# Performance work log

Measured on AMD Instinct MI355X. Metric: run time of the kernel, lower is better.

## Reference

```python
import jax, jax.numpy as jnp
import numpy as np

N_NODES = 100000
N_EDGES = 1600000
NEG_SLOPE = 0.2  # PyG GATConv default


def setup_inputs() -> dict:
    key = jax.random.key(0)
    ks = jax.random.split(key, 10)
    return {
        "x": jax.random.normal(ks[0], (N_NODES, 128), dtype=jnp.float32),
        "edge_index": jax.random.randint(ks[1], (2, N_EDGES), 0, N_NODES, dtype=jnp.int64),
        "W1": jax.random.normal(ks[2], (128, 128), dtype=jnp.float32) * 0.1,
        "a_src1": jax.random.normal(ks[3], (4, 32), dtype=jnp.float32) * 0.1,
        "a_dst1": jax.random.normal(ks[4], (4, 32), dtype=jnp.float32) * 0.1,
        "b1": jax.random.normal(ks[5], (128,), dtype=jnp.float32) * 0.1,
        "W2": jax.random.normal(ks[6], (128, 16), dtype=jnp.float32) * 0.1,
        "a_src2": jax.random.normal(ks[7], (1, 16), dtype=jnp.float32) * 0.1,
        "a_dst2": jax.random.normal(ks[8], (1, 16), dtype=jnp.float32) * 0.1,
        "b2": jax.random.normal(ks[9], (16,), dtype=jnp.float32) * 0.1,
    }


def _gat_layer(x, src, dst, W, a_src, a_dst, b, heads):
    # PyG GATConv (concat=True): xw -> per-edge attention -> segment softmax over
    # incoming edges of each target node -> weighted scatter-sum.
    N = x.shape[0]
    H = heads
    C = W.shape[1] // H
    xw = (x @ W).reshape(N, H, C)                      # [N,H,C]
    al = (xw * a_src).sum(-1)                          # [N,H] source term
    ar = (xw * a_dst).sum(-1)                          # [N,H] target term
    e = jax.nn.leaky_relu(al[src] + ar[dst], NEG_SLOPE)  # [E',H]
    emax = jax.ops.segment_max(e, dst, num_segments=N)   # [N,H]
    em = jnp.exp(e - emax[dst])
    denom = jax.ops.segment_sum(em, dst, num_segments=N)
    alpha = em / denom[dst]                            # [E',H]
    out = jax.ops.segment_sum(xw[src] * alpha[:, :, None], dst, num_segments=N)
    return out.reshape(N, H * C) + b


def reference(x, edge_index, W1, a_src1, a_dst1, b1, W2, a_src2, a_dst2, b2):
    N = x.shape[0]
    loop = jnp.arange(N, dtype=edge_index.dtype)
    # PyG GATConv add_self_loops=True
    src = jnp.concatenate([edge_index[0], loop])
    dst = jnp.concatenate([edge_index[1], loop])
    h = jax.nn.relu(_gat_layer(x, src, dst, W1, a_src1, a_dst1, b1, 4))
    # F.dropout(p=0.5, training=self.training): identity in eval mode
    return _gat_layer(h, src, dst, W2, a_src2, a_dst2, b2, 1)
```

## Files before the change

kernel.cpp:

```cpp
#include <hip/hip_runtime.h>
#include <hip/hip_fp16.h>

#define N_NODES 100000
#define N_EDGES 1600000
#define E_TOT   (N_EDGES + N_NODES)
#define NEG_SLOPE 0.2f
#define PART_EPB 4096
#define BSTRIDE 18432
#define NGEMM (N_NODES / 32)
#define NPART ((E_TOT + PART_EPB - 1) / PART_EPB)

using f16x8 = __attribute__((ext_vector_type(8))) _Float16;
using f32x4 = __attribute__((ext_vector_type(4))) float;
union H8 { f16x8 v; _Float16 h[8]; };

__global__ __launch_bounds__(256)
void k_gemm1_part(const float* __restrict__ x, const float* __restrict__ W1,
                  const float* __restrict__ a_src1, const float* __restrict__ a_dst1,
                  const int* __restrict__ ei, int* __restrict__ bcnt, int* __restrict__ pairs,
                  __half* __restrict__ xw1h, float* __restrict__ al1, float* __restrict__ ar1) {
    __shared__ int lcnt[128];
    __shared__ int lbase[128];
    const int t = threadIdx.x;

    if (blockIdx.x >= NGEMM) {
        const int base = ((int)blockIdx.x - NGEMM) * PART_EPB;
        if (t < 128) lcnt[t] = 0;
        __syncthreads();
        int sr[16], dr[16];
#pragma unroll
        for (int u = 0; u < 16; ++u) {
            const int e = base + u * 256 + t;
            if (e < E_TOT) {
                int s, d;
                if (e < N_EDGES) { s = ei[e]; d = ei[N_EDGES + e]; }
                else             { s = d = e - N_EDGES; }
                sr[u] = s; dr[u] = d;
                atomicAdd(&lcnt[d >> 10], 1);
            } else dr[u] = -1;
        }
        __syncthreads();
        if (t < 128) {
            const int c = lcnt[t];
            lbase[t] = (c > 0) ? atomicAdd(&bcnt[t], c) : 0;
            lcnt[t] = 0;
        }
        __syncthreads();
#pragma unroll
        for (int u = 0; u < 16; ++u) {
            if (dr[u] >= 0) {
                const int bk = dr[u] >> 10;
                const int r = atomicAdd(&lcnt[bk], 1);
                pairs[(size_t)bk * BSTRIDE + lbase[bk] + r] = (sr[u] << 10) | (dr[u] & 1023);
            }
        }
        return;
    }

    const int lane = t & 63;
    const int w = t >> 6;
    const int q = lane >> 4;
    const int n15 = lane & 15;
    const int n0 = (int)blockIdx.x * 32;
    const int j0 = (2 * w) * 16 + n15;
    const int j1 = (2 * w + 1) * 16 + n15;

    f32x4 acc00 = {0.f, 0.f, 0.f, 0.f};
    f32x4 acc01 = acc00, acc10 = acc00, acc11 = acc00;

    for (int kt = 0; kt < 4; ++kt) {
        const int k0 = kt * 32 + q * 8;
        H8 A0, A1, B0, B1;
        {
            const float4* p = (const float4*)&x[(size_t)(n0 + n15) * 128 + k0];
            const float4 xa = p[0], xb = p[1];
            A0.h[0] = (_Float16)xa.x; A0.h[1] = (_Float16)xa.y;
            A0.h[2] = (_Float16)xa.z; A0.h[3] = (_Float16)xa.w;
            A0.h[4] = (_Float16)xb.x; A0.h[5] = (_Float16)xb.y;
            A0.h[6] = (_Float16)xb.z; A0.h[7] = (_Float16)xb.w;
        }
        {
            const float4* p = (const float4*)&x[(size_t)(n0 + 16 + n15) * 128 + k0];
            const float4 xa = p[0], xb = p[1];
            A1.h[0] = (_Float16)xa.x; A1.h[1] = (_Float16)xa.y;
            A1.h[2] = (_Float16)xa.z; A1.h[3] = (_Float16)xa.w;
            A1.h[4] = (_Float16)xb.x; A1.h[5] = (_Float16)xb.y;
            A1.h[6] = (_Float16)xb.z; A1.h[7] = (_Float16)xb.w;
        }
#pragma unroll
        for (int i = 0; i < 8; ++i) {
            B0.h[i] = (_Float16)W1[(size_t)(k0 + i) * 128 + j0];
            B1.h[i] = (_Float16)W1[(size_t)(k0 + i) * 128 + j1];
        }
        acc00 = __builtin_amdgcn_mfma_f32_16x16x32_f16(A0.v, B0.v, acc00, 0, 0, 0);
        acc01 = __builtin_amdgcn_mfma_f32_16x16x32_f16(A0.v, B1.v, acc01, 0, 0, 0);
        acc10 = __builtin_amdgcn_mfma_f32_16x16x32_f16(A1.v, B0.v, acc10, 0, 0, 0);
        acc11 = __builtin_amdgcn_mfma_f32_16x16x32_f16(A1.v, B1.v, acc11, 0, 0, 0);
    }

    const float as0 = a_src1[j0], as1 = a_src1[j1];
    const float ad0 = a_dst1[j0], ad1 = a_dst1[j1];
#pragma unroll
    for (int ng = 0; ng < 2; ++ng) {
        const f32x4 accA = ng ? acc10 : acc00;
        const f32x4 accB = ng ? acc11 : acc01;
#pragma unroll
        for (int r = 0; r < 4; ++r) {
            const int node = n0 + ng * 16 + q * 4 + r;
            xw1h[(size_t)node * 128 + j0] = __float2half(accA[r]);
            xw1h[(size_t)node * 128 + j1] = __float2half(accB[r]);
            float ps = accA[r] * as0 + accB[r] * as1;
            float pd = accA[r] * ad0 + accB[r] * ad1;
#pragma unroll
            for (int o = 1; o < 16; o <<= 1) {
                ps += __shfl_xor(ps, o, 64);
                pd += __shfl_xor(pd, o, 64);
            }
            if (n15 == 0) {
                al1[(size_t)node * 4 + w] = ps;
                ar1[(size_t)node * 4 + w] = pd;
            }
        }
    }
}

__global__ __launch_bounds__(1024)
void k_fill3(const int* __restrict__ pairs, const int* __restrict__ bcnt,
             int* __restrict__ ioff, int* __restrict__ deg, int* __restrict__ ssrc) {
    const int bucket = blockIdx.x;
    const int t = threadIdx.x;
    const int cnt = bcnt[bucket];
    __shared__ int lhist[1024];
    __shared__ int lcur[1024];
    __shared__ int wsum[16];
    __shared__ int sbase;
    lhist[t] = 0;
    if (t == 0) {
        int b = 0;
        for (int k = 0; k < bucket; ++k) b += bcnt[k];
        sbase = b;
    }
    __syncthreads();
    for (int i = t; i < cnt; i += 1024) {
        const int p = pairs[(size_t)bucket * BSTRIDE + i];
        atomicAdd(&lhist[p & 1023], 1);
    }
    __syncthreads();
    const int v = lhist[t];
    int inc = v;
    const int lane = t & 63, wid = t >> 6;
#pragma unroll
    for (int o = 1; o < 64; o <<= 1) {
        const int nv = __shfl_up(inc, o, 64);
        if (lane >= o) inc += nv;
    }
    if (lane == 63) wsum[wid] = inc;
    __syncthreads();
    if (t == 0) {
        int acc = 0;
#pragma unroll
        for (int k = 0; k < 16; ++k) { const int tv = wsum[k]; wsum[k] = acc; acc += tv; }
    }
    __syncthreads();
    const int gofs = sbase + (inc - v) + wsum[wid];
    const int d = bucket * 1024 + t;
    if (d < N_NODES) { ioff[d] = gofs; deg[d] = v; }
    lcur[t] = gofs;
    __syncthreads();
    for (int i = t; i < cnt; i += 1024) {
        const int p = pairs[(size_t)bucket * BSTRIDE + i];
        const int pos = atomicAdd(&lcur[p & 1023], 1);
        ssrc[pos] = p >> 10;
    }
}

__global__ __launch_bounds__(256)
void k_aggr1(const int* __restrict__ ssrc, const int* __restrict__ offs,
             const int* __restrict__ deg, const float* __restrict__ al1,
             const float* __restrict__ ar1, const __half* __restrict__ xw1h,
             const float* __restrict__ b1, __half* __restrict__ out1h) {
    const int lane = threadIdx.x & 63;
    const int d = blockIdx.x * 4 + (threadIdx.x >> 6);
    const int g = lane >> 4;
    const int c = lane & 15;
    const int h = c >> 2;
    const int beg = offs[d];
    const int n = deg[d];
    const float arh = ar1[(size_t)d * 4 + h];
    float acc[8] = {0.f, 0.f, 0.f, 0.f, 0.f, 0.f, 0.f, 0.f};
    float dnm = 0.f;

    for (int base = 0; base < n; base += 8) {
#pragma unroll
        for (int u = 0; u < 2; ++u) {
            const int e = base + u * 4 + g;
            const bool p = e < n;
            const int s = ssrc[beg + (p ? e : 0)];
            float v = al1[(size_t)s * 4 + h] + arh;
            v = v > 0.f ? v : NEG_SLOPE * v;
            const float w = p ? __expf(v) : 0.f;
            const uint4 rv = *(const uint4*)&xw1h[(size_t)s * 128 + c * 8];
            const float2 f0 = __half22float2(*(const __half2*)&rv.x);
            const float2 f1 = __half22float2(*(const __half2*)&rv.y);
            const float2 f2 = __half22float2(*(const __half2*)&rv.z);
            const float2 f3 = __half22float2(*(const __half2*)&rv.w);
            acc[0] = fmaf(w, f0.x, acc[0]); acc[1] = fmaf(w, f0.y, acc[1]);
            acc[2] = fmaf(w, f1.x, acc[2]); acc[3] = fmaf(w, f1.y, acc[3]);
            acc[4] = fmaf(w, f2.x, acc[4]); acc[5] = fmaf(w, f2.y, acc[5]);
            acc[6] = fmaf(w, f3.x, acc[6]); acc[7] = fmaf(w, f3.y, acc[7]);
            dnm += w;
        }
    }
#pragma unroll
    for (int i = 0; i < 8; ++i) {
        acc[i] += __shfl_xor(acc[i], 16, 64);
        acc[i] += __shfl_xor(acc[i], 32, 64);
    }
    dnm += __shfl_xor(dnm, 16, 64);
    dnm += __shfl_xor(dnm, 32, 64);
    if (g == 0) {
        const float rc = 1.f / dnm;
        const float4 b01 = *(const float4*)&b1[c * 8];
        const float4 b23 = *(const float4*)&b1[c * 8 + 4];
        const float bb[8] = {b01.x, b01.y, b01.z, b01.w, b23.x, b23.y, b23.z, b23.w};
        __half ho[8];
#pragma unroll
        for (int i = 0; i < 8; ++i) {
            const float hv = acc[i] * rc + bb[i];
            ho[i] = __float2half(hv > 0.f ? hv : 0.f);
        }
        *(uint4*)&out1h[(size_t)d * 128 + c * 8] = *(uint4*)ho;
    }
}

__global__ __launch_bounds__(256)
void k_gemm2(const __half* __restrict__ out1h, const float* __restrict__ W2,
             const float* __restrict__ a_src2, const float* __restrict__ a_dst2,
             __half* __restrict__ xw2h, float* __restrict__ al2, float* __restrict__ ar2) {
    const int t = threadIdx.x;
    const int node0 = blockIdx.x * 16;
    __shared__ float sW[128 * 16];
    __shared__ float sh[16][129];
    for (int i = t; i < 2048; i += 256) sW[i] = W2[i];
    for (int i = t; i < 2048; i += 256) {
        const int nn = i >> 7, kk = i & 127;
        sh[nn][kk] = __half2float(out1h[(size_t)(node0 + nn) * 128 + kk]);
    }
    __syncthreads();
    const int nn = t >> 4;
    const int j = t & 15;
    float acc = 0.f;
#pragma unroll 8
    for (int k = 0; k < 128; ++k)
        acc = fmaf(sh[nn][k], sW[k * 16 + j], acc);
    xw2h[(size_t)(node0 + nn) * 16 + j] = __float2half(acc);

    float ps = acc * a_src2[j];
    float pd = acc * a_dst2[j];
#pragma unroll
    for (int o = 8; o; o >>= 1) { ps += __shfl_xor(ps, o, 64); pd += __shfl_xor(pd, o, 64); }
    if (j == 0) { al2[node0 + nn] = ps; ar2[node0 + nn] = pd; }
}

__global__ __launch_bounds__(256)
void k_aggr2(const int* __restrict__ ssrc, const int* __restrict__ offs,
             const int* __restrict__ deg, const float* __restrict__ al2,
             const float* __restrict__ ar2, const __half* __restrict__ xw2h,
             const float* __restrict__ b2, float* __restrict__ out) {
    const int lane = threadIdx.x & 63;
    const int node = blockIdx.x * 4 + (threadIdx.x >> 6);
    const int j2 = lane & 7;
    const int eL = lane >> 3;
    const int beg = offs[node];
    const int n = deg[node];
    const float ard = ar2[node];
    float a0 = 0.f, a1 = 0.f, dnm = 0.f;
    for (int base = 0; base < n; base += 16) {
#pragma unroll
        for (int u = 0; u < 2; ++u) {
            const int e = base + u * 8 + eL;
            const bool p = e < n;
            const int s = ssrc[beg + (p ? e : 0)];
            float v = al2[s] + ard;
            v = v > 0.f ? v : NEG_SLOPE * v;
            const float w = p ? __expf(v) : 0.f;
            const float2 f = __half22float2(*(const __half2*)&xw2h[(size_t)s * 16 + j2 * 2]);
            a0 = fmaf(w, f.x, a0);
            a1 = fmaf(w, f.y, a1);
            dnm += w;
        }
    }
#pragma unroll
    for (int o = 8; o < 64; o <<= 1) {
        a0 += __shfl_xor(a0, o, 64);
        a1 += __shfl_xor(a1, o, 64);
        dnm += __shfl_xor(dnm, o, 64);
    }
    if (eL == 0) {
        out[(size_t)node * 16 + j2 * 2]     = a0 / dnm + b2[j2 * 2];
        out[(size_t)node * 16 + j2 * 2 + 1] = a1 / dnm + b2[j2 * 2 + 1];
    }
}

extern "C" void kernel_launch(void* const* d_in, const int* in_sizes, int n_in,
                              void* d_out, int out_size, void* d_ws, size_t ws_size,
                              hipStream_t stream) {
    const float* x      = (const float*)d_in[0];
    const int*   ei     = (const int*)d_in[1];
    const float* W1     = (const float*)d_in[2];
    const float* a_src1 = (const float*)d_in[3];
    const float* a_dst1 = (const float*)d_in[4];
    const float* b1     = (const float*)d_in[5];
    const float* W2     = (const float*)d_in[6];
    const float* a_src2 = (const float*)d_in[7];
    const float* a_dst2 = (const float*)d_in[8];
    const float* b2     = (const float*)d_in[9];
    float* out = (float*)d_out;

    char* wsb = (char*)d_ws;
    __half* xw1h = (__half*)wsb;
    __half* xw2h = (__half*)wsb;
    float*  al2  = (float*)(wsb + (size_t)N_NODES * 16 * 2);
    float*  ar2  = al2 + N_NODES;
    __half* out1h = (__half*)(wsb + (size_t)N_NODES * 128 * 2);
    int*    pairs = (int*)out1h;
    float*  al1  = (float*)(wsb + (size_t)N_NODES * 128 * 4);
    float*  ar1  = al1 + (size_t)N_NODES * 4;
    int* ibcnt = (int*)(ar1 + (size_t)N_NODES * 4);
    int* ioff  = ibcnt + 128;
    int* ideg  = ioff + N_NODES;
    int* isrc  = ideg + N_NODES;

    hipMemsetAsync(ibcnt, 0, 128 * sizeof(int), stream);

    k_gemm1_part<<<NGEMM + NPART, 256, 0, stream>>>(x, W1, a_src1, a_dst1,
                                                    ei, ibcnt, pairs, xw1h, al1, ar1);
    k_fill3<<<128, 1024, 0, stream>>>(pairs, ibcnt, ioff, ideg, isrc);

    k_aggr1<<<N_NODES / 4, 256, 0, stream>>>(isrc, ioff, ideg, al1, ar1, xw1h, b1, out1h);

    k_gemm2<<<N_NODES / 16, 256, 0, stream>>>(out1h, W2, a_src2, a_dst2, xw2h, al2, ar2);
    k_aggr2<<<N_NODES / 4, 256, 0, stream>>>(isrc, ioff, ideg, al2, ar2, xw2h, b2, out);
}
```

Before: 338.7 us.

## Fuse layer-2 projection into layer-1 aggregation and cache bucket counts in LDS

The layer-2 linear transform (h @ W2) and its attention dot products are computed inside the layer-1 aggregation kernel from the registers holding each node's activations, using shuffle reductions across the wavefront. This removes the fp16 out1h intermediate, its global write and re-read, and one kernel launch. The workspace is re-laid out so xw2h/al2/ar2 live in the freed region. The fill kernel also stages bucket counts in shared memory before the serial prefix sum. In exchange every wavefront now does extra W2 loads and shuffles per node.

```diff
diff --git a/kernel.cpp b/kernel.cpp
--- a/kernel.cpp
+++ b/kernel.cpp
@@ -133,14 +133,16 @@
     __shared__ int lhist[1024];
     __shared__ int lcur[1024];
     __shared__ int wsum[16];
+    __shared__ int sbc[128];
     __shared__ int sbase;
     lhist[t] = 0;
+    if (t < 128) sbc[t] = bcnt[t];
+    __syncthreads();
     if (t == 0) {
         int b = 0;
-        for (int k = 0; k < bucket; ++k) b += bcnt[k];
+        for (int k = 0; k < bucket; ++k) b += sbc[k];
         sbase = b;
     }
-    __syncthreads();
     for (int i = t; i < cnt; i += 1024) {
         const int p = pairs[(size_t)bucket * BSTRIDE + i];
         atomicAdd(&lhist[p & 1023], 1);
@@ -178,7 +180,9 @@
 void k_aggr1(const int* __restrict__ ssrc, const int* __restrict__ offs,
              const int* __restrict__ deg, const float* __restrict__ al1,
              const float* __restrict__ ar1, const __half* __restrict__ xw1h,
-             const float* __restrict__ b1, __half* __restrict__ out1h) {
+             const float* __restrict__ b1, const float* __restrict__ W2,
+             const float* __restrict__ a_src2, const float* __restrict__ a_dst2,
+             __half* __restrict__ xw2h, float* __restrict__ al2, float* __restrict__ ar2) {
     const int lane = threadIdx.x & 63;
     const int d = blockIdx.x * 4 + (threadIdx.x >> 6);
     const int g = lane >> 4;
@@ -218,48 +222,45 @@
     }
     dnm += __shfl_xor(dnm, 16, 64);
     dnm += __shfl_xor(dnm, 32, 64);
-    if (g == 0) {
-        const float rc = 1.f / dnm;
-        const float4 b01 = *(const float4*)&b1[c * 8];
-        const float4 b23 = *(const float4*)&b1[c * 8 + 4];
-        const float bb[8] = {b01.x, b01.y, b01.z, b01.w, b23.x, b23.y, b23.z, b23.w};
-        __half ho[8];
-#pragma unroll
-        for (int i = 0; i < 8; ++i) {
-            const float hv = acc[i] * rc + bb[i];
-            ho[i] = __float2half(hv > 0.f ? hv : 0.f);
-        }
-        *(uint4*)&out1h[(size_t)d * 128 + c * 8] = *(uint4*)ho;
-    }
-}
-
-__global__ __launch_bounds__(256)
-void k_gemm2(const __half* __restrict__ out1h, const float* __restrict__ W2,
-             const float* __restrict__ a_src2, const float* __restrict__ a_dst2,
-             __half* __restrict__ xw2h, float* __restrict__ al2, float* __restrict__ ar2) {
-    const int t = threadIdx.x;
-    const int node0 = blockIdx.x * 16;
-    __shared__ float sW[128 * 16];
-    __shared__ float sh[16][129];
-    for (int i = t; i < 2048; i += 256) sW[i] = W2[i];
-    for (int i = t; i < 2048; i += 256) {
-        const int nn = i >> 7, kk = i & 127;
-        sh[nn][kk] = __half2float(out1h[(size_t)(node0 + nn) * 128 + kk]);
-    }
-    __syncthreads();
-    const int nn = t >> 4;
-    const int j = t & 15;
-    float acc = 0.f;
-#pragma unroll 8
-    for (int k = 0; k < 128; ++k)
-        acc = fmaf(sh[nn][k], sW[k * 16 + j], acc);
-    xw2h[(size_t)(node0 + nn) * 16 + j] = __float2half(acc);
-
-    float ps = acc * a_src2[j];
-    float pd = acc * a_dst2[j];
-#pragma unroll
-    for (int o = 8; o; o >>= 1) { ps += __shfl_xor(ps, o, 64); pd += __shfl_xor(pd, o, 64); }
-    if (j == 0) { al2[node0 + nn] = ps; ar2[node0 + nn] = pd; }
+
+    const float rc = 1.f / dnm;
+    const float4 b01 = *(const float4*)&b1[c * 8];
+    const float4 b23 = *(const float4*)&b1[c * 8 + 4];
+    const float bb[8] = {b01.x, b01.y, b01.z, b01.w, b23.x, b23.y, b23.z, b23.w};
+    float hh[8];
+#pragma unroll
+    for (int i = 0; i < 8; ++i) {
+        const float hv = acc[i] * rc + bb[i];
+        hh[i] = hv > 0.f ? hv : 0.f;
+    }
+    float pj0 = 0.f, pj1 = 0.f, pj2 = 0.f, pj3 = 0.f;
+#pragma unroll
+    for (int i = 0; i < 8; ++i) {
+        const float4 wr = *(const float4*)&W2[(size_t)(c * 8 + i) * 16 + g * 4];
+        pj0 = fmaf(hh[i], wr.x, pj0);
+        pj1 = fmaf(hh[i], wr.y, pj1);
+        pj2 = fmaf(hh[i], wr.z, pj2);
+        pj3 = fmaf(hh[i], wr.w, pj3);
+    }
+#pragma unroll
+    for (int o = 1; o < 16; o <<= 1) {
+        pj0 += __shfl_xor(pj0, o, 64);
+        pj1 += __shfl_xor(pj1, o, 64);
+        pj2 += __shfl_xor(pj2, o, 64);
+        pj3 += __shfl_xor(pj3, o, 64);
+    }
+    if (c == 0) {
+        __half hj[4] = {__float2half(pj0), __float2half(pj1),
+                        __float2half(pj2), __float2half(pj3)};
+        *(uint2*)&xw2h[(size_t)d * 16 + g * 4] = *(const uint2*)hj;
+    }
+    const float4 as2 = *(const float4*)&a_src2[g * 4];
+    const float4 ad2 = *(const float4*)&a_dst2[g * 4];
+    float ps2 = pj0 * as2.x + pj1 * as2.y + pj2 * as2.z + pj3 * as2.w;
+    float pd2 = pj0 * ad2.x + pj1 * ad2.y + pj2 * ad2.z + pj3 * ad2.w;
+    ps2 += __shfl_xor(ps2, 16, 64); ps2 += __shfl_xor(ps2, 32, 64);
+    pd2 += __shfl_xor(pd2, 16, 64); pd2 += __shfl_xor(pd2, 32, 64);
+    if (lane == 0) { al2[d] = ps2; ar2[d] = pd2; }
 }
 
 __global__ __launch_bounds__(256)
@@ -319,11 +320,11 @@
 
     char* wsb = (char*)d_ws;
     __half* xw1h = (__half*)wsb;
-    __half* xw2h = (__half*)wsb;
-    float*  al2  = (float*)(wsb + (size_t)N_NODES * 16 * 2);
-    float*  ar2  = al2 + N_NODES;
-    __half* out1h = (__half*)(wsb + (size_t)N_NODES * 128 * 2);
-    int*    pairs = (int*)out1h;
+    char* region2 = wsb + (size_t)N_NODES * 128 * 2;
+    int*    pairs = (int*)region2;
+    __half* xw2h  = (__half*)region2;
+    float*  al2   = (float*)(region2 + (size_t)N_NODES * 16 * 2);
+    float*  ar2   = al2 + N_NODES;
     float*  al1  = (float*)(wsb + (size_t)N_NODES * 128 * 4);
     float*  ar1  = al1 + (size_t)N_NODES * 4;
     int* ibcnt = (int*)(ar1 + (size_t)N_NODES * 4);
@@ -337,8 +338,8 @@
                                                     ei, ibcnt, pairs, xw1h, al1, ar1);
     k_fill3<<<128, 1024, 0, stream>>>(pairs, ibcnt, ioff, ideg, isrc);
 
-    k_aggr1<<<N_NODES / 4, 256, 0, stream>>>(isrc, ioff, ideg, al1, ar1, xw1h, b1, out1h);
-
-    k_gemm2<<<N_NODES / 16, 256, 0, stream>>>(out1h, W2, a_src2, a_dst2, xw2h, al2, ar2);
+    k_aggr1<<<N_NODES / 4, 256, 0, stream>>>(isrc, ioff, ideg, al1, ar1, xw1h, b1,
+                                             W2, a_src2, a_dst2, xw2h, al2, ar2);
+
     k_aggr2<<<N_NODES / 4, 256, 0, stream>>>(isrc, ioff, ideg, al2, ar2, xw2h, b2, out);
 }
```

Result: slower. 363.3 us (+7.3%).
